# Kernel tuning notes

Hardware: AMD Instinct MI355X
Metric: run time of the kernel (lower is better)

The kernel has to match this reference:

```python
import jax, jax.numpy as jnp
import numpy as np

N = 2708
IN_CH = 1433
OUT_CH = 128
NEG_SLOPE = 0.2


def setup_inputs() -> dict:
    key = jax.random.key(0)
    ks = jax.random.split(key, 7)
    X = jax.random.normal(ks[0], (N, IN_CH), dtype=jnp.float32)
    A = jax.random.randint(ks[1], (N, N), 0, 2, dtype=jnp.int32)
    U = jax.random.normal(ks[2], (N, N), dtype=jnp.float32)
    W = jax.random.normal(ks[3], (OUT_CH, IN_CH), dtype=jnp.float32) * (1.0 / np.sqrt(IN_CH))
    a1 = jax.random.normal(ks[4], (1, OUT_CH), dtype=jnp.float32) * (1.0 / np.sqrt(OUT_CH))
    a2 = jax.random.normal(ks[5], (1, OUT_CH), dtype=jnp.float32) * (1.0 / np.sqrt(OUT_CH))
    lmbd = jax.random.normal(ks[6], (N, 1), dtype=jnp.float32)
    return {"X": X, "A": A, "U": U, "W": W, "a1": a1, "a2": a2, "lmbd": lmbd}


def reference(X, A, U, W, a1, a2, lmbd):
    # K = W(X): [N, out]
    K = X @ W.T
    k1 = K @ a1.T                      # [N, 1]
    k2 = K @ a2.T                      # [N, 1]
    E = k1 + k2.T                      # [N, N] broadcast sum
    # spectral filter: igft(lmbd * gft(E)) = U @ (lmbd * (U^T @ E))
    E = jnp.abs(U @ (lmbd * (U.T @ E)))
    E = jnp.where(E >= 0, E, NEG_SLOPE * E)  # leaky_relu
    E_masked = jnp.where(A == 0, -jnp.inf, E)
    alpha = jax.nn.softmax(E_masked, axis=-1)  # row-wise masked softmax
    # dropout p=0.0 (eval) -> identity
    H = alpha @ K                      # [N, out]
    return H
```

## Files before the change

kernel.cpp:

```cpp
#include <hip/hip_runtime.h>
#include <math.h>

#define NN 2708
#define IC 1433
#define OC 128
#define NV (NN / 4)
#define NNOC ((size_t)NN * OC)
#define NW 85

__global__ __launch_bounds__(256) void prep(const int* __restrict__ A, unsigned* __restrict__ bm,
                                            double* __restrict__ zd, int nzd,
                                            const float* __restrict__ W, float* __restrict__ Wt,
                                            const float* __restrict__ a1, const float* __restrict__ a2,
                                            double* __restrict__ w1, double* __restrict__ w2) {
  __shared__ float tile[32][33];
  const int b = blockIdx.x, t = threadIdx.x;
  if (b < 900) {
    int gid = b * 256 + t;
    if (gid < nzd) zd[gid] = 0.0;
    const int total = NN * NW;
    if (gid >= total) return;
    int i = gid / NW, w = gid - i * NW;
    const int* Ar = A + (size_t)i * NN + w * 32;
    unsigned word = 0;
    if (w < NW - 1) {
      const int4* a4 = (const int4*)Ar;
#pragma unroll
      for (int u = 0; u < 8; u++) {
        int4 a = a4[u];
        word |= (a.x != 0 ? 1u : 0u) << (4 * u);
        word |= (a.y != 0 ? 1u : 0u) << (4 * u + 1);
        word |= (a.z != 0 ? 1u : 0u) << (4 * u + 2);
        word |= (a.w != 0 ? 1u : 0u) << (4 * u + 3);
      }
    } else {
      const int nbits = NN - w * 32;
      for (int bb = 0; bb < nbits; bb++) word |= (Ar[bb] != 0 ? 1u : 0u) << bb;
    }
    bm[(size_t)i * NW + w] = word;
  } else if (b < 1080) {
    const int idx = b - 900;
    const int k0 = (idx % 45) * 32, o0 = (idx / 45) * 32;
#pragma unroll
    for (int it = 0; it < 4; it++) {
      int ro = (t >> 5) + it * 8;
      int k  = k0 + (t & 31);
      tile[ro][t & 31] = (k < IC) ? W[(size_t)(o0 + ro) * IC + k] : 0.f;
    }
    __syncthreads();
#pragma unroll
    for (int it = 0; it < 4; it++) {
      int rk = (t >> 5) + it * 8;
      int k  = k0 + rk;
      if (k < IC) Wt[(size_t)k * OC + o0 + (t & 31)] = tile[t & 31][rk];
    }
  } else {
    float* a1s = &tile[0][0];
    float* a2s = a1s + 128;
    if (t < 128) { a1s[t] = a1[t]; a2s[t] = a2[t]; }
    __syncthreads();
    int c = (b - 1080) * 256 + t;
    if (c < IC) {
      const float* Wc = W + c;
      double s1 = 0.0, s2 = 0.0;
#pragma unroll 4
      for (int o = 0; o < OC; o++) {
        double w = (double)Wc[(size_t)o * IC];
        s1 = fma(w, (double)a1s[o], s1);
        s2 = fma(w, (double)a2s[o], s2);
      }
      w1[c] = s1; w2[c] = s2;
    }
  }
}

__global__ __launch_bounds__(256) void xw_gemm(const float* __restrict__ X,
                                               const double* __restrict__ w1, const double* __restrict__ w2,
                                               double* __restrict__ k1, double* __restrict__ k2,
                                               const float* __restrict__ Wt, float* __restrict__ Kp,
                                               int chunk) {
  __shared__ __align__(16) char smem[23040];
  const int b = blockIdx.x, t = threadIdx.x;
  if (b < NN / 4) {
    double* w1s = (double*)smem;
    double* w2s = w1s + IC;
    for (int c = t; c < IC; c += 256) { w1s[c] = w1[c]; w2s[c] = w2[c]; }
    __syncthreads();
    const int wave = t >> 6, lane = t & 63;
    const int i = b * 4 + wave;
    const float* Xi = X + (size_t)i * IC;
    double s1 = 0.0, s2 = 0.0;
    for (int c = lane; c < IC; c += 64) {
      double x = (double)Xi[c];
      s1 = fma(x, w1s[c], s1);
      s2 = fma(x, w2s[c], s2);
    }
    for (int o = 32; o; o >>= 1) { s1 += __shfl_down(s1, o, 64); s2 += __shfl_down(s2, o, 64); }
    if (lane == 0) { k1[i] = s1; k2[i] = s2; }
  } else {
    float (*Xs)[36]  = (float (*)[36])smem;
    float (*Ws)[132] = (float (*)[132])(smem + 32 * 36 * 4);
    const int bb = b - NN / 4;
    const int bx = bb % 85, by = bb / 85;
    const int rb = bx * 32;
    const int ks = by * chunk;
    const int ke = min(IC, ks + chunk);
    float* __restrict__ Ko = Kp + (size_t)by * NNOC;
    const int row0 = (t >> 5) * 4;
    const int col4 = (t & 31) * 4;
    float acc[4][4];
#pragma unroll
    for (int r = 0; r < 4; r++)
#pragma unroll
      for (int c = 0; c < 4; c++) acc[r][c] = 0.f;

    for (int kb = ks; kb < ke; kb += 32) {
#pragma unroll
      for (int it = 0; it < 4; it++) {
        int idx = t + it * 256;
        int r = idx >> 5, c = idx & 31;
        int gr = rb + r, gc = kb + c;
        Xs[r][c] = (gr < NN && gc < ke) ? X[(size_t)gr * IC + gc] : 0.f;
      }
#pragma unroll
      for (int it = 0; it < 4; it++) {
        int idx4 = t + it * 256;
        int k = idx4 >> 5, cg = (idx4 & 31) * 4;
        int gk = kb + k;
        float4 v = make_float4(0.f, 0.f, 0.f, 0.f);
        if (gk < ke) v = *reinterpret_cast<const float4*>(&Wt[(size_t)gk * OC + cg]);
        *reinterpret_cast<float4*>(&Ws[k][cg]) = v;
      }
      __syncthreads();
#pragma unroll
      for (int g = 0; g < 8; g++) {
        float xr[4][4];
#pragma unroll
        for (int r = 0; r < 4; r++)
          *reinterpret_cast<float4*>(xr[r]) = *reinterpret_cast<const float4*>(&Xs[row0 + r][g * 4]);
#pragma unroll
        for (int j = 0; j < 4; j++) {
          const float4 w4 = *reinterpret_cast<const float4*>(&Ws[g * 4 + j][col4]);
#pragma unroll
          for (int r = 0; r < 4; r++) {
            acc[r][0] = fmaf(xr[r][j], w4.x, acc[r][0]);
            acc[r][1] = fmaf(xr[r][j], w4.y, acc[r][1]);
            acc[r][2] = fmaf(xr[r][j], w4.z, acc[r][2]);
            acc[r][3] = fmaf(xr[r][j], w4.w, acc[r][3]);
          }
        }
      }
      __syncthreads();
    }
#pragma unroll
    for (int r = 0; r < 4; r++) {
      int gr = rb + row0 + r;
      if (gr < NN) {
        float4 v = make_float4(acc[r][0], acc[r][1], acc[r][2], acc[r][3]);
        *reinterpret_cast<float4*>(&Ko[(size_t)gr * OC + col4]) = v;
      }
    }
  }
}

__global__ __launch_bounds__(256) void mid(const float4* __restrict__ U4, const double* __restrict__ k1,
                                           double* __restrict__ u1, double* __restrict__ s,
                                           const float4* __restrict__ Kp4, float4* __restrict__ Kf4,
                                           int nsplit) {
  const int b = blockIdx.x, t = threadIdx.x;
  if (b < 255) {
    const int slab = b / 3, chunk = b - slab * 3;
    const int c4 = chunk * 256 + t;
    if (c4 >= NV) return;
    const int r0 = slab * 32;
    const int r1 = min(NN, r0 + 32);
    double au0 = 0, au1_ = 0, au2 = 0, au3 = 0, as0 = 0, as1 = 0, as2 = 0, as3 = 0;
#pragma unroll 4
    for (int r = r0; r < r1; r++) {
      float4 u = U4[(size_t)r * NV + c4];
      double kr = k1[r];
      au0 = fma((double)u.x, kr, au0); au1_ = fma((double)u.y, kr, au1_);
      au2 = fma((double)u.z, kr, au2); au3 = fma((double)u.w, kr, au3);
      as0 += (double)u.x; as1 += (double)u.y; as2 += (double)u.z; as3 += (double)u.w;
    }
    int c = c4 * 4;
    atomicAdd(&u1[c + 0], au0); atomicAdd(&u1[c + 1], au1_);
    atomicAdd(&u1[c + 2], au2); atomicAdd(&u1[c + 3], au3);
    atomicAdd(&s[c + 0], as0);  atomicAdd(&s[c + 1], as1);
    atomicAdd(&s[c + 2], as2);  atomicAdd(&s[c + 3], as3);
  } else {
    size_t i = (size_t)(b - 255) * 256 + t;
    const size_t n4 = NNOC / 4;
    if (i >= n4) return;
    float4 sv;
    if (nsplit == 16) {
      float4 v[16];
#pragma unroll
      for (int pp = 0; pp < 16; pp++) v[pp] = Kp4[(size_t)pp * n4 + i];
      sv = v[0];
#pragma unroll
      for (int pp = 1; pp < 16; pp++) {
        sv.x += v[pp].x; sv.y += v[pp].y; sv.z += v[pp].z; sv.w += v[pp].w;
      }
    } else if (nsplit == 8) {
      float4 v[8];
#pragma unroll
      for (int pp = 0; pp < 8; pp++) v[pp] = Kp4[(size_t)pp * n4 + i];
      sv = v[0];
#pragma unroll
      for (int pp = 1; pp < 8; pp++) {
        sv.x += v[pp].x; sv.y += v[pp].y; sv.z += v[pp].z; sv.w += v[pp].w;
      }
    } else {
      sv = Kp4[i];
      for (int pp = 1; pp < nsplit; pp++) {
        float4 v = Kp4[(size_t)pp * n4 + i];
        sv.x += v.x; sv.y += v.y; sv.z += v.z; sv.w += v.w;
      }
    }
    Kf4[i] = sv;
  }
}

__global__ __launch_bounds__(256) void uv_kernel(const float4* __restrict__ U4, const float4* __restrict__ L4,
                                                 const double2* __restrict__ u1d, const double2* __restrict__ sd,
                                                 double* __restrict__ p, double* __restrict__ q) {
  const int t = threadIdx.x;
  const int wave = t >> 6, lane = t & 63;
  const int r = blockIdx.x * 4 + wave;
  if (r >= NN) return;
  const float4* Ur = U4 + (size_t)r * NV;
  double ap = 0.0, aq = 0.0;
  for (int c4 = lane; c4 < NV; c4 += 64) {
    float4 u = Ur[c4];
    float4 lm = L4[c4];
    double2 ua = u1d[c4 * 2], ub = u1d[c4 * 2 + 1];
    double2 sa = sd[c4 * 2],  sb = sd[c4 * 2 + 1];
    ap = fma((double)u.x, (double)lm.x * ua.x, ap);
    ap = fma((double)u.y, (double)lm.y * ua.y, ap);
    ap = fma((double)u.z, (double)lm.z * ub.x, ap);
    ap = fma((double)u.w, (double)lm.w * ub.y, ap);
    aq = fma((double)u.x, (double)lm.x * sa.x, aq);
    aq = fma((double)u.y, (double)lm.y * sa.y, aq);
    aq = fma((double)u.z, (double)lm.z * sb.x, aq);
    aq = fma((double)u.w, (double)lm.w * sb.y, aq);
  }
  for (int o = 32; o; o >>= 1) { ap += __shfl_down(ap, o, 64); aq += __shfl_down(aq, o, 64); }
  if (lane == 0) { p[r] = ap; q[r] = aq; }
}

__global__ __launch_bounds__(256) void softmaxH_fused(const unsigned* __restrict__ bm,
                                                      const double* __restrict__ p, const double* __restrict__ q,
                                                      const double* __restrict__ k2,
                                                      const float* __restrict__ K, float* __restrict__ H) {
  __shared__ float vf[NN];
  __shared__ short js[NN];
  __shared__ float hpart[4][128];
  __shared__ unsigned bmr[NW];
  __shared__ double redd[4];
  __shared__ float redf[4];
  __shared__ int cntS;

  const int i = blockIdx.x;
  const int t = threadIdx.x;
  const int wv = t >> 6, lane = t & 63;
  const double pi = p[i], qi = q[i];

  if (t < NW) bmr[t] = bm[(size_t)i * NW + t];
  if (t == 0) cntS = 0;
  __syncthreads();

  double m = -1e300;
  for (int j = t; j < NN; j += 256) {
    if ((bmr[j >> 5] >> (j & 31)) & 1u) {
      double v = fma(qi, k2[j], pi);
      m = fmax(m, fabs(v));
    }
  }
  for (int o = 32; o; o >>= 1) m = fmax(m, __shfl_xor(m, o, 64));
  if (lane == 0) redd[wv] = m;
  __syncthreads();
  m = fmax(fmax(redd[0], redd[1]), fmax(redd[2], redd[3]));

  const double thr = m - 21.0;
  const unsigned long long ltmask = (1ull << lane) - 1ull;
  float sw = 0.f;
  for (int j = t; j < NN; j += 256) {
    bool keep = false;
    double av = 0.0;
    if ((bmr[j >> 5] >> (j & 31)) & 1u) {
      av = fabs(fma(qi, k2[j], pi));
      keep = (av > thr);
    }
    unsigned long long mask = __ballot(keep);
    if (mask) {
      int src = __ffsll(mask) - 1;
      int basew = 0;
      if (lane == src) basew = atomicAdd(&cntS, __popcll(mask));
      basew = __shfl(basew, src, 64);
      if (keep) {
        int pos = basew + __popcll(mask & ltmask);
        float w = __expf((float)(av - m));
        js[pos] = (short)j;
        vf[pos] = w;
        sw += w;
      }
    }
  }
  for (int o = 32; o; o >>= 1) sw += __shfl_xor(sw, o, 64);
  if (lane == 0) redf[wv] = sw;
  __syncthreads();
  const float sumw = (redf[0] + redf[1]) + (redf[2] + redf[3]);
  const int nlist = cntS;

  const int ch = t & 63, g = t >> 6;
  float a0 = 0.f, a1 = 0.f;
  int c = g;
  for (; c + 28 < nlist; c += 32) {
    float wr[8]; int jr[8];
#pragma unroll
    for (int u = 0; u < 8; u++) { wr[u] = vf[c + 4 * u]; jr[u] = js[c + 4 * u]; }
    float kl[8], kh[8];
#pragma unroll
    for (int u = 0; u < 8; u++) {
      const float* Kr = K + (size_t)jr[u] * OC;
      kl[u] = Kr[ch]; kh[u] = Kr[64 + ch];
    }
#pragma unroll
    for (int u = 0; u < 8; u++) { a0 = fmaf(wr[u], kl[u], a0); a1 = fmaf(wr[u], kh[u], a1); }
  }
  for (; c < nlist; c += 4) {
    float w = vf[c];
    const float* Kr = K + (size_t)js[c] * OC;
    a0 = fmaf(w, Kr[ch], a0);
    a1 = fmaf(w, Kr[64 + ch], a1);
  }
  hpart[g][ch] = a0;
  hpart[g][64 + ch] = a1;
  __syncthreads();
  if (t < 128) {
    float hv = (hpart[0][t] + hpart[1][t]) + (hpart[2][t] + hpart[3][t]);
    H[(size_t)i * OC + t] = hv / sumw;
  }
}

extern "C" void kernel_launch(void* const* d_in, const int* in_sizes, int n_in,
                              void* d_out, int out_size, void* d_ws, size_t ws_size,
                              hipStream_t stream) {
  const float* X    = (const float*)d_in[0];
  const int*   A    = (const int*)d_in[1];
  const float* U    = (const float*)d_in[2];
  const float* W    = (const float*)d_in[3];
  const float* a1   = (const float*)d_in[4];
  const float* a2   = (const float*)d_in[5];
  const float* lmbd = (const float*)d_in[6];
  float* H = (float*)d_out;

  const size_t wt_bytes  = (size_t)IC * OC * 4;
  const size_t bm_bytes  = (size_t)NN * NW * 4;
  const size_t dbl_bytes = (size_t)(6 * NN + 2 * IC) * 8;

  const int splits[5] = {16, 8, 4, 2, 1};
  int nsplit = 1;
  for (int ci = 0; ci < 5; ci++) {
    int ns = splits[ci];
    size_t need = (size_t)(ns > 1 ? ns + 1 : 1) * NNOC * 4 + wt_bytes + dbl_bytes +
                  bm_bytes + 1024;
    if (need <= ws_size) { nsplit = ns; break; }
  }

  char* base = (char*)d_ws;
  float* Kp = (float*)base;
  float* Kf = (nsplit > 1) ? (float*)(base + (size_t)nsplit * NNOC * 4) : Kp;
  size_t off = (size_t)(nsplit > 1 ? nsplit + 1 : 1) * NNOC * 4;
  float* Wt = (float*)(base + off);            off += wt_bytes;
  double* dbl = (double*)(base + off);         off += dbl_bytes;
  double* k1  = dbl;
  double* k2  = k1 + NN;
  double* u1  = k2 + NN;
  double* sC  = u1 + NN;
  double* p   = sC + NN;
  double* q   = p  + NN;
  double* w1  = q  + NN;
  double* w2  = w1 + IC;
  unsigned* bm = (unsigned*)(base + off);      off += bm_bytes;

  const int chunk = (IC + nsplit - 1) / nsplit;
  const int nmerge = (int)((NNOC / 4 + 255) / 256);

  prep<<<1086, 256, 0, stream>>>(A, bm, u1, 2 * NN, W, Wt, a1, a2, w1, w2);
  xw_gemm<<<677 + 85 * nsplit, 256, 0, stream>>>(X, w1, w2, k1, k2, Wt, Kp, chunk);
  mid<<<255 + (nsplit > 1 ? nmerge : 0), 256, 0, stream>>>((const float4*)U, k1, u1, sC,
                                                           (const float4*)Kp, (float4*)Kf, nsplit);
  uv_kernel<<<NN / 4, 256, 0, stream>>>((const float4*)U, (const float4*)lmbd,
                                        (const double2*)u1, (const double2*)sC, p, q);
  softmaxH_fused<<<NN, 256, 0, stream>>>(bm, p, q, k2, Kf, H);
}
```

Baseline: 207.9 us.

## Fuse five kernels into one persistent cooperative kernel with grid syncs

Merges prep, GEMM, mid, uv and softmax kernels into a single persistent kernel that loops over task indices and separates stages with cooperative grid-wide barriers. It also moves the bitmask and zeroing work out of the first stage into the GEMM stage, so the first stage is much shorter. The aim is to remove four kernel launch boundaries and their drain/fill gaps. In exchange, each stage is limited to occupancy-bounded resident blocks, the shared-memory union may lower occupancy, and grid syncs add their own cost. A fallback to per-phase launches is kept if the cooperative launch fails.

```diff
diff --git a/kernel.cpp b/kernel.cpp
--- a/kernel.cpp
+++ b/kernel.cpp
@@ -1,5 +1,8 @@
 #include <hip/hip_runtime.h>
+#include <hip/hip_cooperative_groups.h>
 #include <math.h>
+
+namespace cg = cooperative_groups;
 
 #define NN 2708
 #define IC 1433
@@ -7,348 +10,388 @@
 #define NV (NN / 4)
 #define NNOC ((size_t)NN * OC)
 #define NW 85
-
-__global__ __launch_bounds__(256) void prep(const int* __restrict__ A, unsigned* __restrict__ bm,
-                                            double* __restrict__ zd, int nzd,
-                                            const float* __restrict__ W, float* __restrict__ Wt,
-                                            const float* __restrict__ a1, const float* __restrict__ a2,
-                                            double* __restrict__ w1, double* __restrict__ w2) {
-  __shared__ float tile[32][33];
-  const int b = blockIdx.x, t = threadIdx.x;
-  if (b < 900) {
-    int gid = b * 256 + t;
-    if (gid < nzd) zd[gid] = 0.0;
-    const int total = NN * NW;
-    if (gid >= total) return;
-    int i = gid / NW, w = gid - i * NW;
-    const int* Ar = A + (size_t)i * NN + w * 32;
-    unsigned word = 0;
-    if (w < NW - 1) {
-      const int4* a4 = (const int4*)Ar;
-#pragma unroll
-      for (int u = 0; u < 8; u++) {
-        int4 a = a4[u];
-        word |= (a.x != 0 ? 1u : 0u) << (4 * u);
-        word |= (a.y != 0 ? 1u : 0u) << (4 * u + 1);
-        word |= (a.z != 0 ? 1u : 0u) << (4 * u + 2);
-        word |= (a.w != 0 ? 1u : 0u) << (4 * u + 3);
-      }
-    } else {
-      const int nbits = NN - w * 32;
-      for (int bb = 0; bb < nbits; bb++) word |= (Ar[bb] != 0 ? 1u : 0u) << bb;
+#define NMERGE 339
+
+struct __align__(16) SMem {
+  union {
+    float tile[32][33];
+    char bsm[23040];
+    struct {
+      float vf[NN];
+      short js[NN];
+      float hpart[4][128];
+      unsigned bmr[NW];
+      double redd[4];
+      float redf[4];
+      int cntS;
+    } e;
+  } u;
+};
+
+__global__ __launch_bounds__(256) void fused(
+    const int* __restrict__ A, unsigned* __restrict__ bm,
+    const float* __restrict__ W, float* __restrict__ Wt,
+    const float* __restrict__ a1v, const float* __restrict__ a2v,
+    double* __restrict__ w1, double* __restrict__ w2,
+    const float* __restrict__ X,
+    double* __restrict__ k1, double* __restrict__ k2,
+    float* __restrict__ Kp, float* __restrict__ Kf,
+    const float* __restrict__ U, const float* __restrict__ lmbd,
+    double* __restrict__ u1, double* __restrict__ sC,
+    double* __restrict__ p, double* __restrict__ q,
+    float* __restrict__ H,
+    int nsplit, int chunk, int phase) {
+  __shared__ SMem sm;
+  const int t = threadIdx.x;
+  const bool coop = (phase < 0);
+
+  if (coop || phase == 0) {
+    for (int tk = blockIdx.x; tk < 186; tk += gridDim.x) {
+      if (tk < 180) {
+        const int k0 = (tk % 45) * 32, o0 = (tk / 45) * 32;
+#pragma unroll
+        for (int it = 0; it < 4; it++) {
+          int ro = (t >> 5) + it * 8;
+          int k  = k0 + (t & 31);
+          sm.u.tile[ro][t & 31] = (k < IC) ? W[(size_t)(o0 + ro) * IC + k] : 0.f;
+        }
+        __syncthreads();
+#pragma unroll
+        for (int it = 0; it < 4; it++) {
+          int rk = (t >> 5) + it * 8;
+          int k  = k0 + rk;
+          if (k < IC) Wt[(size_t)k * OC + o0 + (t & 31)] = sm.u.tile[t & 31][rk];
+        }
+      } else {
+        float* a1s = &sm.u.tile[0][0];
+        float* a2s = a1s + 128;
+        if (t < 128) { a1s[t] = a1v[t]; a2s[t] = a2v[t]; }
+        __syncthreads();
+        int c = (tk - 180) * 256 + t;
+        if (c < IC) {
+          const float* Wc = W + c;
+          double s1 = 0.0, s2 = 0.0;
+#pragma unroll 4
+          for (int o = 0; o < OC; o++) {
+            double wv = (double)Wc[(size_t)o * IC];
+            s1 = fma(wv, (double)a1s[o], s1);
+            s2 = fma(wv, (double)a2s[o], s2);
+          }
+          w1[c] = s1; w2[c] = s2;
+        }
+      }
+      __syncthreads();
     }
-    bm[(size_t)i * NW + w] = word;
-  } else if (b < 1080) {
-    const int idx = b - 900;
-    const int k0 = (idx % 45) * 32, o0 = (idx / 45) * 32;
-#pragma unroll
-    for (int it = 0; it < 4; it++) {
-      int ro = (t >> 5) + it * 8;
-      int k  = k0 + (t & 31);
-      tile[ro][t & 31] = (k < IC) ? W[(size_t)(o0 + ro) * IC + k] : 0.f;
+  }
+  if (coop) cg::this_grid().sync();
+
+  if (coop || phase == 1) {
+    const int ngm = 85 * nsplit;
+    const int ntask = 677 + ngm + 900;
+    for (int tk = blockIdx.x; tk < ntask; tk += gridDim.x) {
+      if (tk < 677) {
+        double* w1s = (double*)sm.u.bsm;
+        double* w2s = w1s + IC;
+        for (int c = t; c < IC; c += 256) { w1s[c] = w1[c]; w2s[c] = w2[c]; }
+        __syncthreads();
+        const int wave = t >> 6, lane = t & 63;
+        const int i = tk * 4 + wave;
+        const float* Xi = X + (size_t)i * IC;
+        double s1 = 0.0, s2 = 0.0;
+        for (int c = lane; c < IC; c += 64) {
+          double x = (double)Xi[c];
+          s1 = fma(x, w1s[c], s1);
+          s2 = fma(x, w2s[c], s2);
+        }
+        for (int o = 32; o; o >>= 1) { s1 += __shfl_down(s1, o, 64); s2 += __shfl_down(s2, o, 64); }
+        if (lane == 0) { k1[i] = s1; k2[i] = s2; }
+      } else if (tk < 677 + ngm) {
+        float (*Xs)[36]  = (float (*)[36])sm.u.bsm;
+        float (*Ws)[132] = (float (*)[132])(sm.u.bsm + 32 * 36 * 4);
+        const int bb = tk - 677;
+        const int bx = bb % 85, by = bb / 85;
+        const int rb = bx * 32;
+        const int ks = by * chunk;
+        const int ke = min(IC, ks + chunk);
+        float* __restrict__ Ko = Kp + (size_t)by * NNOC;
+        const int row0 = (t >> 5) * 4;
+        const int col4 = (t & 31) * 4;
+        float acc[4][4];
+#pragma unroll
+        for (int r = 0; r < 4; r++)
+#pragma unroll
+          for (int c = 0; c < 4; c++) acc[r][c] = 0.f;
+
+        for (int kb = ks; kb < ke; kb += 32) {
+#pragma unroll
+          for (int it = 0; it < 4; it++) {
+            int idx = t + it * 256;
+            int r = idx >> 5, c = idx & 31;
+            int gr = rb + r, gc = kb + c;
+            Xs[r][c] = (gr < NN && gc < ke) ? X[(size_t)gr * IC + gc] : 0.f;
+          }
+#pragma unroll
+          for (int it = 0; it < 4; it++) {
+            int idx4 = t + it * 256;
+            int k = idx4 >> 5, cg2 = (idx4 & 31) * 4;
+            int gk = kb + k;
+            float4 v = make_float4(0.f, 0.f, 0.f, 0.f);
+            if (gk < ke) v = *reinterpret_cast<const float4*>(&Wt[(size_t)gk * OC + cg2]);
+            *reinterpret_cast<float4*>(&Ws[k][cg2]) = v;
+          }
+          __syncthreads();
+#pragma unroll
+          for (int g = 0; g < 8; g++) {
+            float xr[4][4];
+#pragma unroll
+            for (int r = 0; r < 4; r++)
+              *reinterpret_cast<float4*>(xr[r]) = *reinterpret_cast<const float4*>(&Xs[row0 + r][g * 4]);
+#pragma unroll
+            for (int j = 0; j < 4; j++) {
+              const float4 w4 = *reinterpret_cast<const float4*>(&Ws[g * 4 + j][col4]);
+#pragma unroll
+              for (int r = 0; r < 4; r++) {
+                acc[r][0] = fmaf(xr[r][j], w4.x, acc[r][0]);
+                acc[r][1] = fmaf(xr[r][j], w4.y, acc[r][1]);
+                acc[r][2] = fmaf(xr[r][j], w4.z, acc[r][2]);
+                acc[r][3] = fmaf(xr[r][j], w4.w, acc[r][3]);
+              }
+            }
+          }
+          __syncthreads();
+        }
+#pragma unroll
+        for (int r = 0; r < 4; r++) {
+          int gr = rb + row0 + r;
+          if (gr < NN) {
+            float4 v = make_float4(acc[r][0], acc[r][1], acc[r][2], acc[r][3]);
+            *reinterpret_cast<float4*>(&Ko[(size_t)gr * OC + col4]) = v;
+          }
+        }
+      } else {
+        const int b = tk - 677 - ngm;
+        int gid = b * 256 + t;
+        if (gid < 2 * NN) u1[gid] = 0.0;
+        const int total = NN * NW;
+        if (gid < total) {
+          int i = gid / NW, w = gid - i * NW;
+          const int* Ar = A + (size_t)i * NN + w * 32;
+          unsigned word = 0;
+          if (w < NW - 1) {
+            const int4* a4 = (const int4*)Ar;
+#pragma unroll
+            for (int uu = 0; uu < 8; uu++) {
+              int4 a = a4[uu];
+              word |= (a.x != 0 ? 1u : 0u) << (4 * uu);
+              word |= (a.y != 0 ? 1u : 0u) << (4 * uu + 1);
+              word |= (a.z != 0 ? 1u : 0u) << (4 * uu + 2);
+              word |= (a.w != 0 ? 1u : 0u) << (4 * uu + 3);
+            }
+          } else {
+            const int nbits = NN - w * 32;
+            for (int bb2 = 0; bb2 < nbits; bb2++) word |= (Ar[bb2] != 0 ? 1u : 0u) << bb2;
+          }
+          bm[(size_t)i * NW + w] = word;
+        }
+      }
+      __syncthreads();
     }
-    __syncthreads();
-#pragma unroll
-    for (int it = 0; it < 4; it++) {
-      int rk = (t >> 5) + it * 8;
-      int k  = k0 + rk;
-      if (k < IC) Wt[(size_t)k * OC + o0 + (t & 31)] = tile[t & 31][rk];
+  }
+  if (coop) cg::this_grid().sync();
+
+  if (coop || phase == 2) {
+    const int ntask = 255 + (nsplit > 1 ? NMERGE : 0);
+    for (int tk = blockIdx.x; tk < ntask; tk += gridDim.x) {
+      if (tk < 255) {
+        const int slab = tk / 3, ch = tk - slab * 3;
+        const int c4 = ch * 256 + t;
+        if (c4 < NV) {
+          const float4* U4 = (const float4*)U;
+          const int r0 = slab * 32;
+          const int r1 = min(NN, r0 + 32);
+          double au0 = 0, au1_ = 0, au2 = 0, au3 = 0, as0 = 0, as1 = 0, as2 = 0, as3 = 0;
+#pragma unroll 4
+          for (int r = r0; r < r1; r++) {
+            float4 uu = U4[(size_t)r * NV + c4];
+            double kr = k1[r];
+            au0 = fma((double)uu.x, kr, au0); au1_ = fma((double)uu.y, kr, au1_);
+            au2 = fma((double)uu.z, kr, au2); au3 = fma((double)uu.w, kr, au3);
+            as0 += (double)uu.x; as1 += (double)uu.y; as2 += (double)uu.z; as3 += (double)uu.w;
+          }
+          int c = c4 * 4;
+          atomicAdd(&u1[c + 0], au0); atomicAdd(&u1[c + 1], au1_);
+          atomicAdd(&u1[c + 2], au2); atomicAdd(&u1[c + 3], au3);
+          atomicAdd(&sC[c + 0], as0); atomicAdd(&sC[c + 1], as1);
+          atomicAdd(&sC[c + 2], as2); atomicAdd(&sC[c + 3], as3);
+        }
+      } else {
+        size_t i = (size_t)(tk - 255) * 256 + t;
+        const size_t n4 = NNOC / 4;
+        if (i < n4) {
+          const float4* Kp4 = (const float4*)Kp;
+          float4 sv;
+          if (nsplit == 16) {
+            float4 v[16];
+#pragma unroll
+            for (int pp = 0; pp < 16; pp++) v[pp] = Kp4[(size_t)pp * n4 + i];
+            sv = v[0];
+#pragma unroll
+            for (int pp = 1; pp < 16; pp++) { sv.x += v[pp].x; sv.y += v[pp].y; sv.z += v[pp].z; sv.w += v[pp].w; }
+          } else if (nsplit == 8) {
+            float4 v[8];
+#pragma unroll
+            for (int pp = 0; pp < 8; pp++) v[pp] = Kp4[(size_t)pp * n4 + i];
+            sv = v[0];
+#pragma unroll
+            for (int pp = 1; pp < 8; pp++) { sv.x += v[pp].x; sv.y += v[pp].y; sv.z += v[pp].z; sv.w += v[pp].w; }
+          } else if (nsplit == 4) {
+            float4 v[4];
+#pragma unroll
+            for (int pp = 0; pp < 4; pp++) v[pp] = Kp4[(size_t)pp * n4 + i];
+            sv = v[0];
+#pragma unroll
+            for (int pp = 1; pp < 4; pp++) { sv.x += v[pp].x; sv.y += v[pp].y; sv.z += v[pp].z; sv.w += v[pp].w; }
+          } else {
+            sv = Kp4[i];
+            for (int pp = 1; pp < nsplit; pp++) {
+              float4 v = Kp4[(size_t)pp * n4 + i];
+              sv.x += v.x; sv.y += v.y; sv.z += v.z; sv.w += v.w;
+            }
+          }
+          ((float4*)Kf)[i] = sv;
+        }
+      }
     }
-  } else {
-    float* a1s = &tile[0][0];
-    float* a2s = a1s + 128;
-    if (t < 128) { a1s[t] = a1[t]; a2s[t] = a2[t]; }
-    __syncthreads();
-    int c = (b - 1080) * 256 + t;
-    if (c < IC) {
-      const float* Wc = W + c;
-      double s1 = 0.0, s2 = 0.0;
-#pragma unroll 4
-      for (int o = 0; o < OC; o++) {
-        double w = (double)Wc[(size_t)o * IC];
-        s1 = fma(w, (double)a1s[o], s1);
-        s2 = fma(w, (double)a2s[o], s2);
-      }
-      w1[c] = s1; w2[c] = s2;
+  }
+  if (coop) cg::this_grid().sync();
+
+  if (coop || phase == 3) {
+    const float4* U4 = (const float4*)U;
+    const float4* L4 = (const float4*)lmbd;
+    const double2* u1d = (const double2*)u1;
+    const double2* sd  = (const double2*)sC;
+    for (int tk = blockIdx.x; tk < 677; tk += gridDim.x) {
+      const int wave = t >> 6, lane = t & 63;
+      const int r = tk * 4 + wave;
+      const float4* Ur = U4 + (size_t)r * NV;
+      double ap = 0.0, aq = 0.0;
+      for (int c4 = lane; c4 < NV; c4 += 64) {
+        float4 uu = Ur[c4];
+        float4 lm = L4[c4];
+        double2 ua = u1d[c4 * 2], ub = u1d[c4 * 2 + 1];
+        double2 sa = sd[c4 * 2],  sb = sd[c4 * 2 + 1];
+        ap = fma((double)uu.x, (double)lm.x * ua.x, ap);
+        ap = fma((double)uu.y, (double)lm.y * ua.y, ap);
+        ap = fma((double)uu.z, (double)lm.z * ub.x, ap);
+        ap = fma((double)uu.w, (double)lm.w * ub.y, ap);
+        aq = fma((double)uu.x, (double)lm.x * sa.x, aq);
+        aq = fma((double)uu.y, (double)lm.y * sa.y, aq);
+        aq = fma((double)uu.z, (double)lm.z * sb.x, aq);
+        aq = fma((double)uu.w, (double)lm.w * sb.y, aq);
+      }
+      for (int o = 32; o; o >>= 1) { ap += __shfl_down(ap, o, 64); aq += __shfl_down(aq, o, 64); }
+      if (lane == 0) { p[r] = ap; q[r] = aq; }
     }
   }
-}
-
-__global__ __launch_bounds__(256) void xw_gemm(const float* __restrict__ X,
-                                               const double* __restrict__ w1, const double* __restrict__ w2,
-                                               double* __restrict__ k1, double* __restrict__ k2,
-                                               const float* __restrict__ Wt, float* __restrict__ Kp,
-                                               int chunk) {
-  __shared__ __align__(16) char smem[23040];
-  const int b = blockIdx.x, t = threadIdx.x;
-  if (b < NN / 4) {
-    double* w1s = (double*)smem;
-    double* w2s = w1s + IC;
-    for (int c = t; c < IC; c += 256) { w1s[c] = w1[c]; w2s[c] = w2[c]; }
-    __syncthreads();
-    const int wave = t >> 6, lane = t & 63;
-    const int i = b * 4 + wave;
-    const float* Xi = X + (size_t)i * IC;
-    double s1 = 0.0, s2 = 0.0;
-    for (int c = lane; c < IC; c += 64) {
-      double x = (double)Xi[c];
-      s1 = fma(x, w1s[c], s1);
-      s2 = fma(x, w2s[c], s2);
+  if (coop) cg::this_grid().sync();
+
+  if (coop || phase == 4) {
+    float* vf = sm.u.e.vf;
+    short* js = sm.u.e.js;
+    float (*hpart)[128] = sm.u.e.hpart;
+    unsigned* bmr = sm.u.e.bmr;
+    double* redd = sm.u.e.redd;
+    float* redf = sm.u.e.redf;
+    const int wv = t >> 6, lane = t & 63;
+    const unsigned long long ltmask = (1ull << lane) - 1ull;
+
+    for (int i = blockIdx.x; i < NN; i += gridDim.x) {
+      const double pi = p[i], qi = q[i];
+      if (t < NW) bmr[t] = bm[(size_t)i * NW + t];
+      if (t == 0) sm.u.e.cntS = 0;
+      __syncthreads();
+
+      double m = -1e300;
+      for (int j = t; j < NN; j += 256) {
+        if ((bmr[j >> 5] >> (j & 31)) & 1u) {
+          double v = fma(qi, k2[j], pi);
+          m = fmax(m, fabs(v));
+        }
+      }
+      for (int o = 32; o; o >>= 1) m = fmax(m, __shfl_xor(m, o, 64));
+      if (lane == 0) redd[wv] = m;
+      __syncthreads();
+      m = fmax(fmax(redd[0], redd[1]), fmax(redd[2], redd[3]));
+
+      const double thr = m - 21.0;
+      float sw = 0.f;
+      for (int j = t; j < NN; j += 256) {
+        bool keep = false;
+        double av = 0.0;
+        if ((bmr[j >> 5] >> (j & 31)) & 1u) {
+          av = fabs(fma(qi, k2[j], pi));
+          keep = (av > thr);
+        }
+        unsigned long long mask = __ballot(keep);
+        if (mask) {
+          int src = __ffsll(mask) - 1;
+          int basew = 0;
+          if (lane == src) basew = atomicAdd(&sm.u.e.cntS, __popcll(mask));
+          basew = __shfl(basew, src, 64);
+          if (keep) {
+            int pos = basew + __popcll(mask & ltmask);
+            float w = __expf((float)(av - m));
+            js[pos] = (short)j;
+            vf[pos] = w;
+            sw += w;
+          }
+        }
+      }
+      for (int o = 32; o; o >>= 1) sw += __shfl_xor(sw, o, 64);
+      if (lane == 0) redf[wv] = sw;
+      __syncthreads();
+      const float sumw = (redf[0] + redf[1]) + (redf[2] + redf[3]);
+      const int nlist = sm.u.e.cntS;
+
+      const int ch = t & 63, g = t >> 6;
+      float a0 = 0.f, a1 = 0.f;
+      int c = g;
+      for (; c + 28 < nlist; c += 32) {
+        float wr[8]; int jr[8];
+#pragma unroll
+        for (int uu = 0; uu < 8; uu++) { wr[uu] = vf[c + 4 * uu]; jr[uu] = js[c + 4 * uu]; }
+        float kl[8], kh[8];
+#pragma unroll
+        for (int uu = 0; uu < 8; uu++) {
+          const float* Kr = Kf + (size_t)jr[uu] * OC;
+          kl[uu] = Kr[ch]; kh[uu] = Kr[64 + ch];
+        }
+#pragma unroll
+        for (int uu = 0; uu < 8; uu++) { a0 = fmaf(wr[uu], kl[uu], a0); a1 = fmaf(wr[uu], kh[uu], a1); }
+      }
+      for (; c < nlist; c += 4) {
+        float w = vf[c];
+        const float* Kr = Kf + (size_t)js[c] * OC;
+        a0 = fmaf(w, Kr[ch], a0);
+        a1 = fmaf(w, Kr[64 + ch], a1);
+      }
+      hpart[g][ch] = a0;
+      hpart[g][64 + ch] = a1;
+      __syncthreads();
+      if (t < 128) {
+        float hv = (hpart[0][t] + hpart[1][t]) + (hpart[2][t] + hpart[3][t]);
+        H[(size_t)i * OC + t] = hv / sumw;
+      }
+      __syncthreads();
     }
-    for (int o = 32; o; o >>= 1) { s1 += __shfl_down(s1, o, 64); s2 += __shfl_down(s2, o, 64); }
-    if (lane == 0) { k1[i] = s1; k2[i] = s2; }
-  } else {
-    float (*Xs)[36]  = (float (*)[36])smem;
-    float (*Ws)[132] = (float (*)[132])(smem + 32 * 36 * 4);
-    const int bb = b - NN / 4;
-    const int bx = bb % 85, by = bb / 85;
-    const int rb = bx * 32;
-    const int ks = by * chunk;
-    const int ke = min(IC, ks + chunk);
-    float* __restrict__ Ko = Kp + (size_t)by * NNOC;
-    const int row0 = (t >> 5) * 4;
-    const int col4 = (t & 31) * 4;
-    float acc[4][4];
-#pragma unroll
-    for (int r = 0; r < 4; r++)
-#pragma unroll
-      for (int c = 0; c < 4; c++) acc[r][c] = 0.f;
-
-    for (int kb = ks; kb < ke; kb += 32) {
-#pragma unroll
-      for (int it = 0; it < 4; it++) {
-        int idx = t + it * 256;
-        int r = idx >> 5, c = idx & 31;
-        int gr = rb + r, gc = kb + c;
-        Xs[r][c] = (gr < NN && gc < ke) ? X[(size_t)gr * IC + gc] : 0.f;
-      }
-#pragma unroll
-      for (int it = 0; it < 4; it++) {
-        int idx4 = t + it * 256;
-        int k = idx4 >> 5, cg = (idx4 & 31) * 4;
-        int gk = kb + k;
-        float4 v = make_float4(0.f, 0.f, 0.f, 0.f);
-        if (gk < ke) v = *reinterpret_cast<const float4*>(&Wt[(size_t)gk * OC + cg]);
-        *reinterpret_cast<float4*>(&Ws[k][cg]) = v;
-      }
-      __syncthreads();
-#pragma unroll
-      for (int g = 0; g < 8; g++) {
-        float xr[4][4];
-#pragma unroll
-        for (int r = 0; r < 4; r++)
-          *reinterpret_cast<float4*>(xr[r]) = *reinterpret_cast<const float4*>(&Xs[row0 + r][g * 4]);
-#pragma unroll
-        for (int j = 0; j < 4; j++) {
-          const float4 w4 = *reinterpret_cast<const float4*>(&Ws[g * 4 + j][col4]);
-#pragma unroll
-          for (int r = 0; r < 4; r++) {
-            acc[r][0] = fmaf(xr[r][j], w4.x, acc[r][0]);
-            acc[r][1] = fmaf(xr[r][j], w4.y, acc[r][1]);
-            acc[r][2] = fmaf(xr[r][j], w4.z, acc[r][2]);
-            acc[r][3] = fmaf(xr[r][j], w4.w, acc[r][3]);
-          }
-        }
-      }
-      __syncthreads();
-    }
-#pragma unroll
-    for (int r = 0; r < 4; r++) {
-      int gr = rb + row0 + r;
-      if (gr < NN) {
-        float4 v = make_float4(acc[r][0], acc[r][1], acc[r][2], acc[r][3]);
-        *reinterpret_cast<float4*>(&Ko[(size_t)gr * OC + col4]) = v;
-      }
-    }
-  }
-}
-
-__global__ __launch_bounds__(256) void mid(const float4* __restrict__ U4, const double* __restrict__ k1,
-                                           double* __restrict__ u1, double* __restrict__ s,
-                                           const float4* __restrict__ Kp4, float4* __restrict__ Kf4,
-                                           int nsplit) {
-  const int b = blockIdx.x, t = threadIdx.x;
-  if (b < 255) {
-    const int slab = b / 3, chunk = b - slab * 3;
-    const int c4 = chunk * 256 + t;
-    if (c4 >= NV) return;
-    const int r0 = slab * 32;
-    const int r1 = min(NN, r0 + 32);
-    double au0 = 0, au1_ = 0, au2 = 0, au3 = 0, as0 = 0, as1 = 0, as2 = 0, as3 = 0;
-#pragma unroll 4
-    for (int r = r0; r < r1; r++) {
-      float4 u = U4[(size_t)r * NV + c4];
-      double kr = k1[r];
-      au0 = fma((double)u.x, kr, au0); au1_ = fma((double)u.y, kr, au1_);
-      au2 = fma((double)u.z, kr, au2); au3 = fma((double)u.w, kr, au3);
-      as0 += (double)u.x; as1 += (double)u.y; as2 += (double)u.z; as3 += (double)u.w;
-    }
-    int c = c4 * 4;
-    atomicAdd(&u1[c + 0], au0); atomicAdd(&u1[c + 1], au1_);
-    atomicAdd(&u1[c + 2], au2); atomicAdd(&u1[c + 3], au3);
-    atomicAdd(&s[c + 0], as0);  atomicAdd(&s[c + 1], as1);
-    atomicAdd(&s[c + 2], as2);  atomicAdd(&s[c + 3], as3);
-  } else {
-    size_t i = (size_t)(b - 255) * 256 + t;
-    const size_t n4 = NNOC / 4;
-    if (i >= n4) return;
-    float4 sv;
-    if (nsplit == 16) {
-      float4 v[16];
-#pragma unroll
-      for (int pp = 0; pp < 16; pp++) v[pp] = Kp4[(size_t)pp * n4 + i];
-      sv = v[0];
-#pragma unroll
-      for (int pp = 1; pp < 16; pp++) {
-        sv.x += v[pp].x; sv.y += v[pp].y; sv.z += v[pp].z; sv.w += v[pp].w;
-      }
-    } else if (nsplit == 8) {
-      float4 v[8];
-#pragma unroll
-      for (int pp = 0; pp < 8; pp++) v[pp] = Kp4[(size_t)pp * n4 + i];
-      sv = v[0];
-#pragma unroll
-      for (int pp = 1; pp < 8; pp++) {
-        sv.x += v[pp].x; sv.y += v[pp].y; sv.z += v[pp].z; sv.w += v[pp].w;
-      }
-    } else {
-      sv = Kp4[i];
-      for (int pp = 1; pp < nsplit; pp++) {
-        float4 v = Kp4[(size_t)pp * n4 + i];
-        sv.x += v.x; sv.y += v.y; sv.z += v.z; sv.w += v.w;
-      }
-    }
-    Kf4[i] = sv;
-  }
-}
-
-__global__ __launch_bounds__(256) void uv_kernel(const float4* __restrict__ U4, const float4* __restrict__ L4,
-                                                 const double2* __restrict__ u1d, const double2* __restrict__ sd,
-                                                 double* __restrict__ p, double* __restrict__ q) {
-  const int t = threadIdx.x;
-  const int wave = t >> 6, lane = t & 63;
-  const int r = blockIdx.x * 4 + wave;
-  if (r >= NN) return;
-  const float4* Ur = U4 + (size_t)r * NV;
-  double ap = 0.0, aq = 0.0;
-  for (int c4 = lane; c4 < NV; c4 += 64) {
-    float4 u = Ur[c4];
-    float4 lm = L4[c4];
-    double2 ua = u1d[c4 * 2], ub = u1d[c4 * 2 + 1];
-    double2 sa = sd[c4 * 2],  sb = sd[c4 * 2 + 1];
-    ap = fma((double)u.x, (double)lm.x * ua.x, ap);
-    ap = fma((double)u.y, (double)lm.y * ua.y, ap);
-    ap = fma((double)u.z, (double)lm.z * ub.x, ap);
-    ap = fma((double)u.w, (double)lm.w * ub.y, ap);
-    aq = fma((double)u.x, (double)lm.x * sa.x, aq);
-    aq = fma((double)u.y, (double)lm.y * sa.y, aq);
-    aq = fma((double)u.z, (double)lm.z * sb.x, aq);
-    aq = fma((double)u.w, (double)lm.w * sb.y, aq);
-  }
-  for (int o = 32; o; o >>= 1) { ap += __shfl_down(ap, o, 64); aq += __shfl_down(aq, o, 64); }
-  if (lane == 0) { p[r] = ap; q[r] = aq; }
-}
-
-__global__ __launch_bounds__(256) void softmaxH_fused(const unsigned* __restrict__ bm,
-                                                      const double* __restrict__ p, const double* __restrict__ q,
-                                                      const double* __restrict__ k2,
-                                                      const float* __restrict__ K, float* __restrict__ H) {
-  __shared__ float vf[NN];
-  __shared__ short js[NN];
-  __shared__ float hpart[4][128];
-  __shared__ unsigned bmr[NW];
-  __shared__ double redd[4];
-  __shared__ float redf[4];
-  __shared__ int cntS;
-
-  const int i = blockIdx.x;
-  const int t = threadIdx.x;
-  const int wv = t >> 6, lane = t & 63;
-  const double pi = p[i], qi = q[i];
-
-  if (t < NW) bmr[t] = bm[(size_t)i * NW + t];
-  if (t == 0) cntS = 0;
-  __syncthreads();
-
-  double m = -1e300;
-  for (int j = t; j < NN; j += 256) {
-    if ((bmr[j >> 5] >> (j & 31)) & 1u) {
-      double v = fma(qi, k2[j], pi);
-      m = fmax(m, fabs(v));
-    }
-  }
-  for (int o = 32; o; o >>= 1) m = fmax(m, __shfl_xor(m, o, 64));
-  if (lane == 0) redd[wv] = m;
-  __syncthreads();
-  m = fmax(fmax(redd[0], redd[1]), fmax(redd[2], redd[3]));
-
-  const double thr = m - 21.0;
-  const unsigned long long ltmask = (1ull << lane) - 1ull;
-  float sw = 0.f;
-  for (int j = t; j < NN; j += 256) {
-    bool keep = false;
-    double av = 0.0;
-    if ((bmr[j >> 5] >> (j & 31)) & 1u) {
-      av = fabs(fma(qi, k2[j], pi));
-      keep = (av > thr);
-    }
-    unsigned long long mask = __ballot(keep);
-    if (mask) {
-      int src = __ffsll(mask) - 1;
-      int basew = 0;
-      if (lane == src) basew = atomicAdd(&cntS, __popcll(mask));
-      basew = __shfl(basew, src, 64);
-      if (keep) {
-        int pos = basew + __popcll(mask & ltmask);
-        float w = __expf((float)(av - m));
-        js[pos] = (short)j;
-        vf[pos] = w;
-        sw += w;
-      }
-    }
-  }
-  for (int o = 32; o; o >>= 1) sw += __shfl_xor(sw, o, 64);
-  if (lane == 0) redf[wv] = sw;
-  __syncthreads();
-  const float sumw = (redf[0] + redf[1]) + (redf[2] + redf[3]);
-  const int nlist = cntS;
-
-  const int ch = t & 63, g = t >> 6;
-  float a0 = 0.f, a1 = 0.f;
-  int c = g;
-  for (; c + 28 < nlist; c += 32) {
-    float wr[8]; int jr[8];
-#pragma unroll
-    for (int u = 0; u < 8; u++) { wr[u] = vf[c + 4 * u]; jr[u] = js[c + 4 * u]; }
-    float kl[8], kh[8];
-#pragma unroll
-    for (int u = 0; u < 8; u++) {
-      const float* Kr = K + (size_t)jr[u] * OC;
-      kl[u] = Kr[ch]; kh[u] = Kr[64 + ch];
-    }
-#pragma unroll
-    for (int u = 0; u < 8; u++) { a0 = fmaf(wr[u], kl[u], a0); a1 = fmaf(wr[u], kh[u], a1); }
-  }
-  for (; c < nlist; c += 4) {
-    float w = vf[c];
-    const float* Kr = K + (size_t)js[c] * OC;
-    a0 = fmaf(w, Kr[ch], a0);
-    a1 = fmaf(w, Kr[64 + ch], a1);
-  }
-  hpart[g][ch] = a0;
-  hpart[g][64 + ch] = a1;
-  __syncthreads();
-  if (t < 128) {
-    float hv = (hpart[0][t] + hpart[1][t]) + (hpart[2][t] + hpart[3][t]);
-    H[(size_t)i * OC + t] = hv / sumw;
   }
 }
 
 extern "C" void kernel_launch(void* const* d_in, const int* in_sizes, int n_in,
                               void* d_out, int out_size, void* d_ws, size_t ws_size,
                               hipStream_t stream) {
+  const int*   A    = (const int*)d_in[1];
   const float* X    = (const float*)d_in[0];
-  const int*   A    = (const int*)d_in[1];
   const float* U    = (const float*)d_in[2];
   const float* W    = (const float*)d_in[3];
   const float* a1   = (const float*)d_in[4];
@@ -385,14 +428,39 @@
   double* w2  = w1 + IC;
   unsigned* bm = (unsigned*)(base + off);      off += bm_bytes;
 
-  const int chunk = (IC + nsplit - 1) / nsplit;
-  const int nmerge = (int)((NNOC / 4 + 255) / 256);
-
-  prep<<<1086, 256, 0, stream>>>(A, bm, u1, 2 * NN, W, Wt, a1, a2, w1, w2);
-  xw_gemm<<<677 + 85 * nsplit, 256, 0, stream>>>(X, w1, w2, k1, k2, Wt, Kp, chunk);
-  mid<<<255 + (nsplit > 1 ? nmerge : 0), 256, 0, stream>>>((const float4*)U, k1, u1, sC,
-                                                           (const float4*)Kp, (float4*)Kf, nsplit);
-  uv_kernel<<<NN / 4, 256, 0, stream>>>((const float4*)U, (const float4*)lmbd,
-                                        (const double2*)u1, (const double2*)sC, p, q);
-  softmaxH_fused<<<NN, 256, 0, stream>>>(bm, p, q, k2, Kf, H);
+  int chunk = (IC + nsplit - 1) / nsplit;
+
+  static int nblk_cache = -1;
+  if (nblk_cache < 0) {
+    int occ = 0;
+    if (hipOccupancyMaxActiveBlocksPerMultiprocessor(&occ, fused, 256, 0) != hipSuccess || occ <= 0)
+      occ = 2;
+    int ncu = 256;
+    hipDeviceProp_t prop;
+    if (hipGetDeviceProperties(&prop, 0) == hipSuccess && prop.multiProcessorCount > 0)
+      ncu = prop.multiProcessorCount;
+    nblk_cache = occ * ncu;
+  }
+  int ntask_max = 677 + 85 * nsplit + 900;
+  if (ntask_max < NN) ntask_max = NN;
+  int NBLK = nblk_cache < ntask_max ? nblk_cache : ntask_max;
+
+  int phase = -1;
+  void* args[] = {(void*)&A, (void*)&bm, (void*)&W, (void*)&Wt, (void*)&a1, (void*)&a2,
+                  (void*)&w1, (void*)&w2, (void*)&X, (void*)&k1, (void*)&k2,
+                  (void*)&Kp, (void*)&Kf, (void*)&U, (void*)&lmbd, (void*)&u1, (void*)&sC,
+                  (void*)&p, (void*)&q, (void*)&H, (void*)&nsplit, (void*)&chunk, (void*)&phase};
+  hipError_t err = hipLaunchCooperativeKernel(fused, dim3(NBLK), dim3(256), args, 0, stream);
+  if (err != hipSuccess) {
+    fused<<<186, 256, 0, stream>>>(A, bm, W, Wt, a1, a2, w1, w2, X, k1, k2, Kp, Kf,
+                                   U, lmbd, u1, sC, p, q, H, nsplit, chunk, 0);
+    fused<<<677 + 85 * nsplit + 900, 256, 0, stream>>>(A, bm, W, Wt, a1, a2, w1, w2, X, k1, k2, Kp, Kf,
+                                                       U, lmbd, u1, sC, p, q, H, nsplit, chunk, 1);
+    fused<<<255 + (nsplit > 1 ? NMERGE : 0), 256, 0, stream>>>(A, bm, W, Wt, a1, a2, w1, w2, X, k1, k2, Kp, Kf,
+                                                               U, lmbd, u1, sC, p, q, H, nsplit, chunk, 2);
+    fused<<<677, 256, 0, stream>>>(A, bm, W, Wt, a1, a2, w1, w2, X, k1, k2, Kp, Kf,
+                                   U, lmbd, u1, sC, p, q, H, nsplit, chunk, 3);
+    fused<<<NN, 256, 0, stream>>>(A, bm, W, Wt, a1, a2, w1, w2, X, k1, k2, Kp, Kf,
+                                  U, lmbd, u1, sC, p, q, H, nsplit, chunk, 4);
+  }
 }
```

After: 438.0 us. 2.11x slower.

## Fuse U·v row products into softmax kernel and move bitmask build into GEMM launch

Applied to the files above, without the earlier changes.

The per-row p/q dot products over U (previously a separate uv_kernel writing p and q to global memory) are now computed at the start of each softmax block, one block per row, and reduced through shared memory. The adjacency-bitmask construction moves from the prep kernel into extra blocks of the xw_gemm launch, so prep shrinks to the W transpose, the w1/w2 vectors and the zeroing. This removes one kernel launch and the p/q round trip, and lets the A-to-bitmask conversion overlap the GEMM. The cost is that each softmax block now also streams a full U row with 256 threads before its softmax work, and the GEMM launch gets 900 more blocks.

```diff
diff --git a/kernel.cpp b/kernel.cpp
--- a/kernel.cpp
+++ b/kernel.cpp
@@ -8,39 +8,14 @@
 #define NNOC ((size_t)NN * OC)
 #define NW 85
 
-__global__ __launch_bounds__(256) void prep(const int* __restrict__ A, unsigned* __restrict__ bm,
-                                            double* __restrict__ zd, int nzd,
-                                            const float* __restrict__ W, float* __restrict__ Wt,
-                                            const float* __restrict__ a1, const float* __restrict__ a2,
-                                            double* __restrict__ w1, double* __restrict__ w2) {
+__global__ __launch_bounds__(256) void prep2(const float* __restrict__ W, float* __restrict__ Wt,
+                                             const float* __restrict__ a1, const float* __restrict__ a2,
+                                             double* __restrict__ w1, double* __restrict__ w2,
+                                             double* __restrict__ zd, int nzd) {
   __shared__ float tile[32][33];
   const int b = blockIdx.x, t = threadIdx.x;
-  if (b < 900) {
-    int gid = b * 256 + t;
-    if (gid < nzd) zd[gid] = 0.0;
-    const int total = NN * NW;
-    if (gid >= total) return;
-    int i = gid / NW, w = gid - i * NW;
-    const int* Ar = A + (size_t)i * NN + w * 32;
-    unsigned word = 0;
-    if (w < NW - 1) {
-      const int4* a4 = (const int4*)Ar;
-#pragma unroll
-      for (int u = 0; u < 8; u++) {
-        int4 a = a4[u];
-        word |= (a.x != 0 ? 1u : 0u) << (4 * u);
-        word |= (a.y != 0 ? 1u : 0u) << (4 * u + 1);
-        word |= (a.z != 0 ? 1u : 0u) << (4 * u + 2);
-        word |= (a.w != 0 ? 1u : 0u) << (4 * u + 3);
-      }
-    } else {
-      const int nbits = NN - w * 32;
-      for (int bb = 0; bb < nbits; bb++) word |= (Ar[bb] != 0 ? 1u : 0u) << bb;
-    }
-    bm[(size_t)i * NW + w] = word;
-  } else if (b < 1080) {
-    const int idx = b - 900;
-    const int k0 = (idx % 45) * 32, o0 = (idx / 45) * 32;
+  if (b < 180) {
+    const int k0 = (b % 45) * 32, o0 = (b / 45) * 32;
 #pragma unroll
     for (int it = 0; it < 4; it++) {
       int ro = (t >> 5) + it * 8;
@@ -54,12 +29,12 @@
       int k  = k0 + rk;
       if (k < IC) Wt[(size_t)k * OC + o0 + (t & 31)] = tile[t & 31][rk];
     }
-  } else {
+  } else if (b < 186) {
     float* a1s = &tile[0][0];
     float* a2s = a1s + 128;
     if (t < 128) { a1s[t] = a1[t]; a2s[t] = a2[t]; }
     __syncthreads();
-    int c = (b - 1080) * 256 + t;
+    int c = (b - 180) * 256 + t;
     if (c < IC) {
       const float* Wc = W + c;
       double s1 = 0.0, s2 = 0.0;
@@ -71,6 +46,9 @@
       }
       w1[c] = s1; w2[c] = s2;
     }
+  } else {
+    int gid = (b - 186) * 256 + t;
+    if (gid < nzd) zd[gid] = 0.0;
   }
 }
 
@@ -78,9 +56,11 @@
                                                const double* __restrict__ w1, const double* __restrict__ w2,
                                                double* __restrict__ k1, double* __restrict__ k2,
                                                const float* __restrict__ Wt, float* __restrict__ Kp,
-                                               int chunk) {
+                                               const int* __restrict__ A, unsigned* __restrict__ bm,
+                                               int chunk, int nsplit) {
   __shared__ __align__(16) char smem[23040];
   const int b = blockIdx.x, t = threadIdx.x;
+  const int ngm = 85 * nsplit;
   if (b < NN / 4) {
     double* w1s = (double*)smem;
     double* w2s = w1s + IC;
@@ -97,7 +77,7 @@
     }
     for (int o = 32; o; o >>= 1) { s1 += __shfl_down(s1, o, 64); s2 += __shfl_down(s2, o, 64); }
     if (lane == 0) { k1[i] = s1; k2[i] = s2; }
-  } else {
+  } else if (b < NN / 4 + ngm) {
     float (*Xs)[36]  = (float (*)[36])smem;
     float (*Ws)[132] = (float (*)[132])(smem + 32 * 36 * 4);
     const int bb = b - NN / 4;
@@ -160,6 +140,29 @@
         *reinterpret_cast<float4*>(&Ko[(size_t)gr * OC + col4]) = v;
       }
     }
+  } else {
+    const int bb = b - NN / 4 - ngm;
+    int gid = bb * 256 + t;
+    const int total = NN * NW;
+    if (gid >= total) return;
+    int i = gid / NW, w = gid - i * NW;
+    const int* Ar = A + (size_t)i * NN + w * 32;
+    unsigned word = 0;
+    if (w < NW - 1) {
+      const int4* a4 = (const int4*)Ar;
+#pragma unroll
+      for (int u = 0; u < 8; u++) {
+        int4 a = a4[u];
+        word |= (a.x != 0 ? 1u : 0u) << (4 * u);
+        word |= (a.y != 0 ? 1u : 0u) << (4 * u + 1);
+        word |= (a.z != 0 ? 1u : 0u) << (4 * u + 2);
+        word |= (a.w != 0 ? 1u : 0u) << (4 * u + 3);
+      }
+    } else {
+      const int nbits = NN - w * 32;
+      for (int bb2 = 0; bb2 < nbits; bb2++) word |= (Ar[bb2] != 0 ? 1u : 0u) << bb2;
+    }
+    bm[(size_t)i * NW + w] = word;
   }
 }
 
@@ -222,16 +225,30 @@
   }
 }
 
-__global__ __launch_bounds__(256) void uv_kernel(const float4* __restrict__ U4, const float4* __restrict__ L4,
-                                                 const double2* __restrict__ u1d, const double2* __restrict__ sd,
-                                                 double* __restrict__ p, double* __restrict__ q) {
+__global__ __launch_bounds__(256) void softuvH(const unsigned* __restrict__ bm,
+                                               const float4* __restrict__ U4, const float4* __restrict__ L4,
+                                               const double2* __restrict__ u1d, const double2* __restrict__ sd,
+                                               const double* __restrict__ k2,
+                                               const float* __restrict__ K, float* __restrict__ H) {
+  __shared__ float vf[NN];
+  __shared__ short js[NN];
+  __shared__ float hpart[4][128];
+  __shared__ unsigned bmr[NW];
+  __shared__ double redd[4], redp[4], redq[4];
+  __shared__ float redf[4];
+  __shared__ int cntS;
+
+  const int i = blockIdx.x;
   const int t = threadIdx.x;
-  const int wave = t >> 6, lane = t & 63;
-  const int r = blockIdx.x * 4 + wave;
-  if (r >= NN) return;
-  const float4* Ur = U4 + (size_t)r * NV;
+  const int wv = t >> 6, lane = t & 63;
+  const unsigned long long ltmask = (1ull << lane) - 1ull;
+
+  if (t < NW) bmr[t] = bm[(size_t)i * NW + t];
+  if (t == 0) cntS = 0;
+
+  const float4* Ur = U4 + (size_t)i * NV;
   double ap = 0.0, aq = 0.0;
-  for (int c4 = lane; c4 < NV; c4 += 64) {
+  for (int c4 = t; c4 < NV; c4 += 256) {
     float4 u = Ur[c4];
     float4 lm = L4[c4];
     double2 ua = u1d[c4 * 2], ub = u1d[c4 * 2 + 1];
@@ -246,29 +263,10 @@
     aq = fma((double)u.w, (double)lm.w * sb.y, aq);
   }
   for (int o = 32; o; o >>= 1) { ap += __shfl_down(ap, o, 64); aq += __shfl_down(aq, o, 64); }
-  if (lane == 0) { p[r] = ap; q[r] = aq; }
-}
-
-__global__ __launch_bounds__(256) void softmaxH_fused(const unsigned* __restrict__ bm,
-                                                      const double* __restrict__ p, const double* __restrict__ q,
-                                                      const double* __restrict__ k2,
-                                                      const float* __restrict__ K, float* __restrict__ H) {
-  __shared__ float vf[NN];
-  __shared__ short js[NN];
-  __shared__ float hpart[4][128];
-  __shared__ unsigned bmr[NW];
-  __shared__ double redd[4];
-  __shared__ float redf[4];
-  __shared__ int cntS;
-
-  const int i = blockIdx.x;
-  const int t = threadIdx.x;
-  const int wv = t >> 6, lane = t & 63;
-  const double pi = p[i], qi = q[i];
-
-  if (t < NW) bmr[t] = bm[(size_t)i * NW + t];
-  if (t == 0) cntS = 0;
+  if (lane == 0) { redp[wv] = ap; redq[wv] = aq; }
   __syncthreads();
+  const double pi = (redp[0] + redp[1]) + (redp[2] + redp[3]);
+  const double qi = (redq[0] + redq[1]) + (redq[2] + redq[3]);
 
   double m = -1e300;
   for (int j = t; j < NN; j += 256) {
@@ -283,7 +281,6 @@
   m = fmax(fmax(redd[0], redd[1]), fmax(redd[2], redd[3]));
 
   const double thr = m - 21.0;
-  const unsigned long long ltmask = (1ull << lane) - 1ull;
   float sw = 0.f;
   for (int j = t; j < NN; j += 256) {
     bool keep = false;
@@ -379,20 +376,18 @@
   double* k2  = k1 + NN;
   double* u1  = k2 + NN;
   double* sC  = u1 + NN;
-  double* p   = sC + NN;
-  double* q   = p  + NN;
-  double* w1  = q  + NN;
+  double* w1  = sC + NN + 2 * NN;
   double* w2  = w1 + IC;
   unsigned* bm = (unsigned*)(base + off);      off += bm_bytes;
 
   const int chunk = (IC + nsplit - 1) / nsplit;
   const int nmerge = (int)((NNOC / 4 + 255) / 256);
 
-  prep<<<1086, 256, 0, stream>>>(A, bm, u1, 2 * NN, W, Wt, a1, a2, w1, w2);
-  xw_gemm<<<677 + 85 * nsplit, 256, 0, stream>>>(X, w1, w2, k1, k2, Wt, Kp, chunk);
+  prep2<<<208, 256, 0, stream>>>(W, Wt, a1, a2, w1, w2, u1, 2 * NN);
+  xw_gemm<<<677 + 85 * nsplit + 900, 256, 0, stream>>>(X, w1, w2, k1, k2, Wt, Kp, A, bm,
+                                                       chunk, nsplit);
   mid<<<255 + (nsplit > 1 ? nmerge : 0), 256, 0, stream>>>((const float4*)U, k1, u1, sC,
                                                            (const float4*)Kp, (float4*)Kf, nsplit);
-  uv_kernel<<<NN / 4, 256, 0, stream>>>((const float4*)U, (const float4*)lmbd,
-                                        (const double2*)u1, (const double2*)sC, p, q);
-  softmaxH_fused<<<NN, 256, 0, stream>>>(bm, p, q, k2, Kf, H);
-}
+  softuvH<<<NN, 256, 0, stream>>>(bm, (const float4*)U, (const float4*)lmbd,
+                                  (const double2*)u1, (const double2*)sC, k2, Kf, H);
+}
```

Result: faster. 202.2 us (-2.7%).
